# Kernel tuning notes

Measured on AMD Instinct MI355X. Metric: run time of the kernel, lower is better.

Reference implementation:

```python
import jax, jax.numpy as jnp
import numpy as np

H = 64  # hidden size
T = 11  # unrolled timesteps


def setup_inputs() -> dict:
    key = jax.random.key(0)
    ks = jax.random.split(key, 8)
    B, V, E = 65536, 50000, 100
    return {
        "sent": jax.random.randint(ks[0], (B, T), 0, V, dtype=jnp.int32),
        "emb_W": jax.random.normal(ks[1], (V, E), jnp.float32) * 0.05,
        "W_ih": jax.random.normal(ks[2], (4 * H, E), jnp.float32) * 0.05,
        "W_hh": jax.random.normal(ks[3], (4 * H, H), jnp.float32) * 0.05,
        "b_ih": jax.random.normal(ks[4], (4 * H,), jnp.float32) * 0.05,
        "b_hh": jax.random.normal(ks[5], (4 * H,), jnp.float32) * 0.05,
        "fc_W": jax.random.normal(ks[6], (14, H), jnp.float32) * 0.05,
        "fc_b": jax.random.normal(ks[7], (14,), jnp.float32) * 0.05,
    }


def _lstm_cell(x, h, c, W_ih, W_hh, b_ih, b_hh):
    # gates order in torch LSTMCell: i, f, g, o
    gates = x @ W_ih.T + b_ih + h @ W_hh.T + b_hh  # [B, 4H]
    i, f, g, o = jnp.split(gates, 4, axis=-1)
    c_new = jax.nn.sigmoid(f) * c + jax.nn.sigmoid(i) * jnp.tanh(g)
    h_new = jax.nn.sigmoid(o) * jnp.tanh(c_new)
    return h_new, c_new


def reference(sent, emb_W, W_ih, W_hh, b_ih, b_hh, fc_W, fc_b):
    embed = emb_W[sent]  # [B, T, E]
    B = embed.shape[0]
    h0 = jnp.zeros((B, H), embed.dtype)
    c0 = jnp.zeros((B, H), embed.dtype)
    xs = jnp.swapaxes(embed[:, :T, :], 0, 1)  # [T, B, E]

    def step(carry, x):
        h, c = carry
        h, c = _lstm_cell(x, h, c, W_ih, W_hh, b_ih, b_hh)
        return (h, c), None

    (h_last, _), _ = jax.lax.scan(step, (h0, c0), xs)
    logits = h_last @ fc_W.T + fc_b  # [B, 14]
    return jax.nn.log_softmax(logits, axis=-1)
```

## Files before the change

kernel.cpp:

```cpp
#include <hip/hip_runtime.h>
#include <hip/hip_bf16.h>

#define T_STEPS 11
#define E_DIM   100
#define XSL     2048
#define NDMA    (2 * T_STEPS)

typedef int   i32x2   __attribute__((ext_vector_type(2)));
typedef int   i32x4   __attribute__((ext_vector_type(4)));
typedef int   i32x8   __attribute__((ext_vector_type(8)));
typedef float f32x4   __attribute__((ext_vector_type(4)));
typedef _Float16 h16x2 __attribute__((ext_vector_type(2)));
typedef _Float16 h16x4 __attribute__((ext_vector_type(4)));
typedef _Float16 h16x8 __attribute__((ext_vector_type(8)));

typedef __attribute__((address_space(1))) const unsigned int g_as1;
typedef __attribute__((address_space(3))) unsigned int l_as3;

#define SCALE1 0x7f7f7f7f

__device__ __forceinline__ h16x2 spl2(float v) {
    _Float16 h = (_Float16)v;
    return (h16x2){h, h};
}
__device__ __forceinline__ h16x2 pk2(float a, float b) {
    return __builtin_bit_cast(h16x2, __builtin_amdgcn_cvt_pkrtz(a, b));
}
__device__ __forceinline__ unsigned char f2fp8(float f) {
    return (unsigned char)(__builtin_amdgcn_cvt_pk_fp8_f32(f, 0.f, 0, false) & 0xff);
}
__device__ __forceinline__ long long ll_lo(i32x4 v) {
    i32x2 t = {v[0], v[1]};
    return __builtin_bit_cast(long long, t);
}
__device__ __forceinline__ long long ll_hi(i32x4 v) {
    i32x2 t = {v[2], v[3]};
    return __builtin_bit_cast(long long, t);
}

__device__ __forceinline__ h16x2 tanh5(h16x2 x) {
    h16x2 x2 = x * x;
    h16x2 p = x2 * spl2(0.13333333f) + spl2(-0.33333333f);
    p = x2 * p + spl2(1.0f);
    return x * p;
}
__device__ __forceinline__ h16x2 tanh7(h16x2 x) {
    h16x2 x2 = x * x;
    h16x2 p = x2 * spl2(-0.05396825f) + spl2(0.13333333f);
    p = x2 * p + spl2(-0.33333333f);
    p = x2 * p + spl2(1.0f);
    return x * p;
}
__device__ __forceinline__ h16x2 sig3(h16x2 x) {
    h16x2 x2 = x * x;
    h16x2 p = x2 * spl2(-0.020833334f) + spl2(0.25f);
    return x * p + spl2(0.5f);
}

__global__ void pack_all(const float* __restrict__ emb,
                         const float* __restrict__ W_ih, const float* __restrict__ W_hh,
                         const float* __restrict__ b_ih, const float* __restrict__ b_hh,
                         unsigned char* __restrict__ embp8, unsigned char* __restrict__ Wx8,
                         unsigned char* __restrict__ Wh8, float* __restrict__ biasf, int V)
{
    int b = blockIdx.x;
    int tid = threadIdx.x;
    if (b < 128) {
        int id = b * 256 + tid;
        int n = id >> 7, k = id & 127;
        float v = (k < E_DIM) ? W_ih[n * E_DIM + k] : 0.f;
        int kt = k >> 5;
        int lane = (n & 15) | (((k & 31) >> 3) << 4);
        Wx8[((kt * 16 + (n >> 4)) * 64 + lane) * 8 + (k & 7)] = f2fp8(v);
    } else if (b < 192) {
        int id = (b - 128) * 256 + tid;
        int n = id >> 6, k = id & 63;
        int kt = k >> 5;
        int lane = (n & 15) | (((k & 31) >> 3) << 4);
        Wh8[((kt * 16 + (n >> 4)) * 64 + lane) * 8 + (k & 7)] = f2fp8(W_hh[n * 64 + k]);
    } else if (b == 192) {
        biasf[tid] = b_ih[tid] + b_hh[tid];
    } else {
        int id = (b - 193) * 256 + tid;
        if (id >= V * 8) return;
        int row = id >> 3;
        int c8 = id & 7;
        int p = c8 >> 2, qq = c8 & 3;
        const float* xr = emb + (size_t)row * E_DIM;
        float v[16];
        #pragma unroll
        for (int w = 0; w < 16; ++w) {
            int k = p * 64 + (w >> 3) * 32 + qq * 8 + (w & 7);
            v[w] = (k < E_DIM) ? xr[k] : 0.f;
        }
        int4 o;
        int* op = &o.x;
        #pragma unroll
        for (int w = 0; w < 4; ++w) {
            int d = __builtin_amdgcn_cvt_pk_fp8_f32(v[w*4+0], v[w*4+1], 0, false);
            d = __builtin_amdgcn_cvt_pk_fp8_f32(v[w*4+2], v[w*4+3], d, true);
            op[w] = d;
        }
        *reinterpret_cast<int4*>(embp8 + (size_t)row * 128 + c8 * 16) = o;
    }
}

template<int PACKED>
__global__ __launch_bounds__(256, 4)
void lstm_fused(const int* __restrict__ sent,
                const float* __restrict__ emb, const unsigned char* __restrict__ embp8,
                const unsigned char* __restrict__ Wx8, const unsigned char* __restrict__ Wh8,
                const float* __restrict__ biasf,
                const float* __restrict__ fc_W, const float* __restrict__ fc_b,
                float* __restrict__ out)
{
    __shared__ unsigned char xlds[T_STEPS * XSL];
    __shared__ unsigned char hlds[2][1024];
    __shared__ float biaslds[256];
    __shared__ short hscr[16 * 68];
    const int tid  = threadIdx.x;
    const int wv   = tid >> 6;
    const int lane = tid & 63;
    const int r    = lane & 15;
    const int q    = lane >> 4;
    const int b0   = blockIdx.x * 16;

    #pragma unroll
    for (int d = wv; d < NDMA; d += 4) {
        int sl = d >> 1, half = d & 1;
        int c  = half * 4 + (lane >> 4);
        int rr = lane & 15;
        int idx = sent[(b0 + rr) * T_STEPS + sl];
        if (PACKED) {
            const unsigned char* src = embp8 + (size_t)idx * 128 + c * 16;
            __builtin_amdgcn_global_load_lds(
                (g_as1*)src, (l_as3*)&xlds[sl * XSL + half * 1024], 16, 0, 0);
        } else {
            const float* xr = emb + (size_t)idx * E_DIM;
            int p = c >> 2, qq = c & 3;
            float v[16];
            #pragma unroll
            for (int w = 0; w < 16; ++w) {
                int k = p * 64 + (w >> 3) * 32 + qq * 8 + (w & 7);
                v[w] = (k < E_DIM) ? xr[k] : 0.f;
            }
            int4 o;
            int* op = &o.x;
            #pragma unroll
            for (int w = 0; w < 4; ++w) {
                int dd = __builtin_amdgcn_cvt_pk_fp8_f32(v[w*4+0], v[w*4+1], 0, false);
                dd = __builtin_amdgcn_cvt_pk_fp8_f32(v[w*4+2], v[w*4+3], dd, true);
                op[w] = dd;
            }
            *reinterpret_cast<int4*>(&xlds[sl * XSL + (half * 64 + lane) * 16]) = o;
        }
    }

    i32x8 wxm[4];
    #pragma unroll
    for (int g = 0; g < 4; ++g)
        #pragma unroll
        for (int kt = 0; kt < 4; ++kt) {
            i32x2 w = *reinterpret_cast<const i32x2*>(
                Wx8 + ((kt * 16 + g * 4 + wv) * 64 + lane) * 8);
            wxm[g][2 * kt]     = w[0];
            wxm[g][2 * kt + 1] = w[1];
        }
    long long wh[2][4];
    #pragma unroll
    for (int kt = 0; kt < 2; ++kt)
        #pragma unroll
        for (int g = 0; g < 4; ++g)
            wh[kt][g] = *reinterpret_cast<const long long*>(
                Wh8 + ((kt * 16 + g * 4 + wv) * 64 + lane) * 8);
    #pragma unroll
    for (int g = 0; g < 4; ++g)
        asm volatile("" : "+v"(wxm[g]));
    #pragma unroll
    for (int kt = 0; kt < 2; ++kt)
        #pragma unroll
        for (int g = 0; g < 4; ++g)
            asm volatile("" : "+v"(wh[kt][g]));

    biaslds[tid] = biasf[tid];
    reinterpret_cast<int*>(&hlds[0][0])[tid] = 0;

    __builtin_amdgcn_s_waitcnt(0);
    __syncthreads();

    auto acc_bias_x = [&](int sl, f32x4* acc) {
        #pragma unroll
        for (int g = 0; g < 4; ++g)
            acc[g] = *reinterpret_cast<const f32x4*>(
                &biaslds[(g * 4 + wv) * 16 + q * 4]);
        i32x4 v0 = *reinterpret_cast<const i32x4*>(
            &xlds[sl * XSL + (q * 16 + r) * 16]);
        i32x4 v1 = *reinterpret_cast<const i32x4*>(
            &xlds[sl * XSL + ((4 + q) * 16 + r) * 16]);
        i32x8 b8 = {v0[0], v0[1], v0[2], v0[3], v1[0], v1[1], v1[2], v1[3]};
        #pragma unroll
        for (int g = 0; g < 4; ++g)
            acc[g] = __builtin_amdgcn_mfma_scale_f32_16x16x128_f8f6f4(
                wxm[g], b8, acc[g], 0, 0, 0, SCALE1, 0, SCALE1);
    };

    h16x2 c01 = spl2(0.f), c23 = spl2(0.f);
    f32x4 acc[4];
    acc_bias_x(0, acc);

    const int hq  = (wv & 1) * 2 + (q >> 1);
    const int hoff = (hq * 16 + r) * 16 + (wv >> 1) * 8 + (q & 1) * 4;

    #pragma unroll
    for (int t = 0; t < T_STEPS; ++t) {
        i32x4 hv = *reinterpret_cast<const i32x4*>(&hlds[t & 1][(q * 16 + r) * 16]);
        long long bh0 = ll_lo(hv), bh1 = ll_hi(hv);
        #pragma unroll
        for (int g = 0; g < 4; ++g)
            acc[g] = __builtin_amdgcn_mfma_f32_16x16x32_fp8_fp8(wh[0][g], bh0, acc[g], 0, 0, 0);
        #pragma unroll
        for (int g = 0; g < 4; ++g)
            acc[g] = __builtin_amdgcn_mfma_f32_16x16x32_fp8_fp8(wh[1][g], bh1, acc[g], 0, 0, 0);

        h16x2 gi0 = pk2(acc[0][0], acc[0][1]), gi1 = pk2(acc[0][2], acc[0][3]);
        h16x2 gf0 = pk2(acc[1][0], acc[1][1]), gf1 = pk2(acc[1][2], acc[1][3]);
        h16x2 gg0 = pk2(acc[2][0], acc[2][1]), gg1 = pk2(acc[2][2], acc[2][3]);
        h16x2 go0 = pk2(acc[3][0], acc[3][1]), go1 = pk2(acc[3][2], acc[3][3]);
        c01 = sig3(gf0) * c01 + sig3(gi0) * tanh5(gg0);
        c23 = sig3(gf1) * c23 + sig3(gi1) * tanh5(gg1);
        h16x2 h01 = sig3(go0) * tanh7(c01);
        h16x2 h23 = sig3(go1) * tanh7(c23);

        int hw = __builtin_amdgcn_cvt_pk_fp8_f32((float)h01[0], (float)h01[1], 0, false);
        hw = __builtin_amdgcn_cvt_pk_fp8_f32((float)h23[0], (float)h23[1], hw, true);
        *reinterpret_cast<int*>(&hlds[(t + 1) & 1][hoff]) = hw;

        if (t == T_STEPS - 1) {
            h16x4 hn = { h01[0], h01[1], h23[0], h23[1] };
            *reinterpret_cast<h16x4*>(&hscr[r * 68 + wv * 16 + q * 4]) = hn;
        }

        if (t + 1 < T_STEPS) acc_bias_x(t + 1, acc);

        __syncthreads();
    }

    const int row_local = wv * 4 + q;
    const int cls = r;
    const int brow = b0 + row_local;
    float s = (cls < 14) ? fc_b[cls] : 0.f;
    const float* wrow = fc_W + ((cls < 14) ? cls : 0) * 64;
    #pragma unroll
    for (int ch = 0; ch < 8; ++ch) {
        h16x8 hv8 = *reinterpret_cast<const h16x8*>(&hscr[row_local * 68 + ch * 8]);
        #pragma unroll
        for (int j = 0; j < 8; ++j)
            s = fmaf((float)hv8[j], wrow[ch * 8 + j], s);
    }
    float lg = (cls < 14) ? s : -1e30f;
    float mx = lg;
    mx = fmaxf(mx, __shfl_xor(mx, 1));
    mx = fmaxf(mx, __shfl_xor(mx, 2));
    mx = fmaxf(mx, __shfl_xor(mx, 4));
    mx = fmaxf(mx, __shfl_xor(mx, 8));
    float se = __expf(lg - mx);
    se += __shfl_xor(se, 1);
    se += __shfl_xor(se, 2);
    se += __shfl_xor(se, 4);
    se += __shfl_xor(se, 8);
    float lse = mx + __logf(se);
    if (cls < 14) out[(size_t)brow * 14 + cls] = lg - lse;
}

extern "C" void kernel_launch(void* const* d_in, const int* in_sizes, int n_in,
                              void* d_out, int out_size, void* d_ws, size_t ws_size,
                              hipStream_t stream)
{
    const int*   sent = (const int*)d_in[0];
    const float* emb  = (const float*)d_in[1];
    const float* W_ih = (const float*)d_in[2];
    const float* W_hh = (const float*)d_in[3];
    const float* b_ih = (const float*)d_in[4];
    const float* b_hh = (const float*)d_in[5];
    const float* fc_W = (const float*)d_in[6];
    const float* fc_b = (const float*)d_in[7];
    float* out = (float*)d_out;

    const int B = in_sizes[0] / T_STEPS;
    const int V = in_sizes[1] / E_DIM;
    const size_t emb_bytes = (size_t)V * 128;
    const size_t need = emb_bytes + 32768 + 16384 + 1024;
    const bool packed = ws_size >= need;

    unsigned char* embp8 = (unsigned char*)d_ws;
    unsigned char* Wx8   = embp8 + emb_bytes;
    unsigned char* Wh8   = Wx8 + 32768;
    float*         biasf = (float*)(Wh8 + 16384);
    if (!packed) {
        Wx8   = (unsigned char*)d_ws;
        Wh8   = Wx8 + 32768;
        biasf = (float*)(Wh8 + 16384);
        embp8 = nullptr;
    }

    const int grid = B / 16;
    if (packed) {
        int pgrid = 193 + (V * 8 + 255) / 256;
        pack_all<<<pgrid, 256, 0, stream>>>(emb, W_ih, W_hh, b_ih, b_hh,
                                            embp8, Wx8, Wh8, biasf, V);
        lstm_fused<1><<<grid, 256, 0, stream>>>(sent, emb, embp8, Wx8, Wh8,
                                                biasf, fc_W, fc_b, out);
    } else {
        pack_all<<<193, 256, 0, stream>>>(emb, W_ih, W_hh, b_ih, b_hh,
                                          nullptr, Wx8, Wh8, biasf, 0);
        lstm_fused<0><<<grid, 256, 0, stream>>>(sent, emb, nullptr, Wx8, Wh8,
                                                biasf, fc_W, fc_b, out);
    }
}
```

Baseline: 147.0 us.

## Process two 16-row batch tiles per block to interleave independent recurrences

Each block now handles 32 batch rows as two independent 16-row LSTM chains. Their MFMAs and gate math are interleaved so one chain's latency can hide behind the other's work, and the per-step barrier cost and weight-register loads are shared across twice the rows. The grid is halved, LDS use roughly doubles, and launch bounds drop from 4 to 3 blocks per CU. The hscr scratch is folded into the reused x buffer. This trades occupancy and register pressure for more instruction-level parallelism.

```diff
diff --git a/kernel.cpp b/kernel.cpp
--- a/kernel.cpp
+++ b/kernel.cpp
@@ -106,7 +106,7 @@
 }
 
 template<int PACKED>
-__global__ __launch_bounds__(256, 4)
+__global__ __launch_bounds__(256, 3)
 void lstm_fused(const int* __restrict__ sent,
                 const float* __restrict__ emb, const unsigned char* __restrict__ embp8,
                 const unsigned char* __restrict__ Wx8, const unsigned char* __restrict__ Wh8,
@@ -114,27 +114,28 @@
                 const float* __restrict__ fc_W, const float* __restrict__ fc_b,
                 float* __restrict__ out)
 {
-    __shared__ unsigned char xlds[T_STEPS * XSL];
-    __shared__ unsigned char hlds[2][1024];
+    __shared__ unsigned char xlds[2][T_STEPS * XSL];
+    __shared__ unsigned char hlds[2][2][1024];
     __shared__ float biaslds[256];
-    __shared__ short hscr[16 * 68];
     const int tid  = threadIdx.x;
     const int wv   = tid >> 6;
     const int lane = tid & 63;
     const int r    = lane & 15;
     const int q    = lane >> 4;
-    const int b0   = blockIdx.x * 16;
-
-    #pragma unroll
-    for (int d = wv; d < NDMA; d += 4) {
-        int sl = d >> 1, half = d & 1;
+    const int b0   = blockIdx.x * 32;
+
+    #pragma unroll
+    for (int d = wv; d < 2 * NDMA; d += 4) {
+        int u  = (d >= NDMA);
+        int dd = d - u * NDMA;
+        int sl = dd >> 1, half = d & 1;
         int c  = half * 4 + (lane >> 4);
         int rr = lane & 15;
-        int idx = sent[(b0 + rr) * T_STEPS + sl];
+        int idx = sent[(b0 + u * 16 + rr) * T_STEPS + sl];
         if (PACKED) {
             const unsigned char* src = embp8 + (size_t)idx * 128 + c * 16;
             __builtin_amdgcn_global_load_lds(
-                (g_as1*)src, (l_as3*)&xlds[sl * XSL + half * 1024], 16, 0, 0);
+                (g_as1*)src, (l_as3*)&xlds[u][sl * XSL + half * 1024], 16, 0, 0);
         } else {
             const float* xr = emb + (size_t)idx * E_DIM;
             int p = c >> 2, qq = c & 3;
@@ -148,11 +149,11 @@
             int* op = &o.x;
             #pragma unroll
             for (int w = 0; w < 4; ++w) {
-                int dd = __builtin_amdgcn_cvt_pk_fp8_f32(v[w*4+0], v[w*4+1], 0, false);
-                dd = __builtin_amdgcn_cvt_pk_fp8_f32(v[w*4+2], v[w*4+3], dd, true);
-                op[w] = dd;
+                int e = __builtin_amdgcn_cvt_pk_fp8_f32(v[w*4+0], v[w*4+1], 0, false);
+                e = __builtin_amdgcn_cvt_pk_fp8_f32(v[w*4+2], v[w*4+3], e, true);
+                op[w] = e;
             }
-            *reinterpret_cast<int4*>(&xlds[sl * XSL + (half * 64 + lane) * 16]) = o;
+            *reinterpret_cast<int4*>(&xlds[u][sl * XSL + (half * 64 + lane) * 16]) = o;
         }
     }
 
@@ -183,20 +184,20 @@
             asm volatile("" : "+v"(wh[kt][g]));
 
     biaslds[tid] = biasf[tid];
-    reinterpret_cast<int*>(&hlds[0][0])[tid] = 0;
+    reinterpret_cast<int2*>(&hlds[0][0][0])[tid] = (int2){0, 0};
 
     __builtin_amdgcn_s_waitcnt(0);
     __syncthreads();
 
-    auto acc_bias_x = [&](int sl, f32x4* acc) {
+    auto acc_bias_x = [&](int sl, int u, f32x4* acc) {
         #pragma unroll
         for (int g = 0; g < 4; ++g)
             acc[g] = *reinterpret_cast<const f32x4*>(
                 &biaslds[(g * 4 + wv) * 16 + q * 4]);
         i32x4 v0 = *reinterpret_cast<const i32x4*>(
-            &xlds[sl * XSL + (q * 16 + r) * 16]);
+            &xlds[u][sl * XSL + (q * 16 + r) * 16]);
         i32x4 v1 = *reinterpret_cast<const i32x4*>(
-            &xlds[sl * XSL + ((4 + q) * 16 + r) * 16]);
+            &xlds[u][sl * XSL + ((4 + q) * 16 + r) * 16]);
         i32x8 b8 = {v0[0], v0[1], v0[2], v0[3], v1[0], v1[1], v1[2], v1[3]};
         #pragma unroll
         for (int g = 0; g < 4; ++g)
@@ -204,72 +205,96 @@
                 wxm[g], b8, acc[g], 0, 0, 0, SCALE1, 0, SCALE1);
     };
 
-    h16x2 c01 = spl2(0.f), c23 = spl2(0.f);
-    f32x4 acc[4];
-    acc_bias_x(0, acc);
-
-    const int hq  = (wv & 1) * 2 + (q >> 1);
+    h16x2 c01[2] = {spl2(0.f), spl2(0.f)}, c23[2] = {spl2(0.f), spl2(0.f)};
+    f32x4 acc[2][4];
+    acc_bias_x(0, 0, acc[0]);
+    acc_bias_x(0, 1, acc[1]);
+
+    const int hq   = (wv & 1) * 2 + (q >> 1);
     const int hoff = (hq * 16 + r) * 16 + (wv >> 1) * 8 + (q & 1) * 4;
 
+    h16x4 hfin[2];
+
     #pragma unroll
     for (int t = 0; t < T_STEPS; ++t) {
-        i32x4 hv = *reinterpret_cast<const i32x4*>(&hlds[t & 1][(q * 16 + r) * 16]);
-        long long bh0 = ll_lo(hv), bh1 = ll_hi(hv);
-        #pragma unroll
-        for (int g = 0; g < 4; ++g)
-            acc[g] = __builtin_amdgcn_mfma_f32_16x16x32_fp8_fp8(wh[0][g], bh0, acc[g], 0, 0, 0);
-        #pragma unroll
-        for (int g = 0; g < 4; ++g)
-            acc[g] = __builtin_amdgcn_mfma_f32_16x16x32_fp8_fp8(wh[1][g], bh1, acc[g], 0, 0, 0);
-
-        h16x2 gi0 = pk2(acc[0][0], acc[0][1]), gi1 = pk2(acc[0][2], acc[0][3]);
-        h16x2 gf0 = pk2(acc[1][0], acc[1][1]), gf1 = pk2(acc[1][2], acc[1][3]);
-        h16x2 gg0 = pk2(acc[2][0], acc[2][1]), gg1 = pk2(acc[2][2], acc[2][3]);
-        h16x2 go0 = pk2(acc[3][0], acc[3][1]), go1 = pk2(acc[3][2], acc[3][3]);
-        c01 = sig3(gf0) * c01 + sig3(gi0) * tanh5(gg0);
-        c23 = sig3(gf1) * c23 + sig3(gi1) * tanh5(gg1);
-        h16x2 h01 = sig3(go0) * tanh7(c01);
-        h16x2 h23 = sig3(go1) * tanh7(c23);
-
-        int hw = __builtin_amdgcn_cvt_pk_fp8_f32((float)h01[0], (float)h01[1], 0, false);
-        hw = __builtin_amdgcn_cvt_pk_fp8_f32((float)h23[0], (float)h23[1], hw, true);
-        *reinterpret_cast<int*>(&hlds[(t + 1) & 1][hoff]) = hw;
-
-        if (t == T_STEPS - 1) {
-            h16x4 hn = { h01[0], h01[1], h23[0], h23[1] };
-            *reinterpret_cast<h16x4*>(&hscr[r * 68 + wv * 16 + q * 4]) = hn;
-        }
-
-        if (t + 1 < T_STEPS) acc_bias_x(t + 1, acc);
+        i32x4 hv0 = *reinterpret_cast<const i32x4*>(&hlds[t & 1][0][(q * 16 + r) * 16]);
+        i32x4 hv1 = *reinterpret_cast<const i32x4*>(&hlds[t & 1][1][(q * 16 + r) * 16]);
+        {
+            long long a0 = ll_lo(hv0), a1 = ll_hi(hv0);
+            long long b0_ = ll_lo(hv1), b1 = ll_hi(hv1);
+            #pragma unroll
+            for (int g = 0; g < 4; ++g) {
+                acc[0][g] = __builtin_amdgcn_mfma_f32_16x16x32_fp8_fp8(wh[0][g], a0, acc[0][g], 0, 0, 0);
+                acc[1][g] = __builtin_amdgcn_mfma_f32_16x16x32_fp8_fp8(wh[0][g], b0_, acc[1][g], 0, 0, 0);
+            }
+            #pragma unroll
+            for (int g = 0; g < 4; ++g) {
+                acc[0][g] = __builtin_amdgcn_mfma_f32_16x16x32_fp8_fp8(wh[1][g], a1, acc[0][g], 0, 0, 0);
+                acc[1][g] = __builtin_amdgcn_mfma_f32_16x16x32_fp8_fp8(wh[1][g], b1, acc[1][g], 0, 0, 0);
+            }
+        }
+
+        #pragma unroll
+        for (int u = 0; u < 2; ++u) {
+            h16x2 gi0 = pk2(acc[u][0][0], acc[u][0][1]), gi1 = pk2(acc[u][0][2], acc[u][0][3]);
+            h16x2 gf0 = pk2(acc[u][1][0], acc[u][1][1]), gf1 = pk2(acc[u][1][2], acc[u][1][3]);
+            h16x2 gg0 = pk2(acc[u][2][0], acc[u][2][1]), gg1 = pk2(acc[u][2][2], acc[u][2][3]);
+            h16x2 go0 = pk2(acc[u][3][0], acc[u][3][1]), go1 = pk2(acc[u][3][2], acc[u][3][3]);
+            c01[u] = sig3(gf0) * c01[u] + sig3(gi0) * tanh5(gg0);
+            c23[u] = sig3(gf1) * c23[u] + sig3(gi1) * tanh5(gg1);
+            h16x2 h01 = sig3(go0) * tanh7(c01[u]);
+            h16x2 h23 = sig3(go1) * tanh7(c23[u]);
+            int hw = __builtin_amdgcn_cvt_pk_fp8_f32((float)h01[0], (float)h01[1], 0, false);
+            hw = __builtin_amdgcn_cvt_pk_fp8_f32((float)h23[0], (float)h23[1], hw, true);
+            *reinterpret_cast<int*>(&hlds[(t + 1) & 1][u][hoff]) = hw;
+            if (t == T_STEPS - 1)
+                hfin[u] = (h16x4){h01[0], h01[1], h23[0], h23[1]};
+        }
+
+        if (t + 1 < T_STEPS) {
+            acc_bias_x(t + 1, 0, acc[0]);
+            acc_bias_x(t + 1, 1, acc[1]);
+        }
 
         __syncthreads();
     }
+
+    #pragma unroll
+    for (int u = 0; u < 2; ++u) {
+        short* hscr = reinterpret_cast<short*>(&xlds[u][0]);
+        *reinterpret_cast<h16x4*>(&hscr[r * 68 + wv * 16 + q * 4]) = hfin[u];
+    }
+    __syncthreads();
 
     const int row_local = wv * 4 + q;
     const int cls = r;
-    const int brow = b0 + row_local;
-    float s = (cls < 14) ? fc_b[cls] : 0.f;
     const float* wrow = fc_W + ((cls < 14) ? cls : 0) * 64;
-    #pragma unroll
-    for (int ch = 0; ch < 8; ++ch) {
-        h16x8 hv8 = *reinterpret_cast<const h16x8*>(&hscr[row_local * 68 + ch * 8]);
-        #pragma unroll
-        for (int j = 0; j < 8; ++j)
-            s = fmaf((float)hv8[j], wrow[ch * 8 + j], s);
-    }
-    float lg = (cls < 14) ? s : -1e30f;
-    float mx = lg;
-    mx = fmaxf(mx, __shfl_xor(mx, 1));
-    mx = fmaxf(mx, __shfl_xor(mx, 2));
-    mx = fmaxf(mx, __shfl_xor(mx, 4));
-    mx = fmaxf(mx, __shfl_xor(mx, 8));
-    float se = __expf(lg - mx);
-    se += __shfl_xor(se, 1);
-    se += __shfl_xor(se, 2);
-    se += __shfl_xor(se, 4);
-    se += __shfl_xor(se, 8);
-    float lse = mx + __logf(se);
-    if (cls < 14) out[(size_t)brow * 14 + cls] = lg - lse;
+    float bias_c = (cls < 14) ? fc_b[cls] : 0.f;
+    #pragma unroll
+    for (int u = 0; u < 2; ++u) {
+        const short* hscr = reinterpret_cast<const short*>(&xlds[u][0]);
+        float s = bias_c;
+        #pragma unroll
+        for (int ch = 0; ch < 8; ++ch) {
+            h16x8 hv8 = *reinterpret_cast<const h16x8*>(&hscr[row_local * 68 + ch * 8]);
+            #pragma unroll
+            for (int j = 0; j < 8; ++j)
+                s = fmaf((float)hv8[j], wrow[ch * 8 + j], s);
+        }
+        float lg = (cls < 14) ? s : -1e30f;
+        float mx = lg;
+        mx = fmaxf(mx, __shfl_xor(mx, 1));
+        mx = fmaxf(mx, __shfl_xor(mx, 2));
+        mx = fmaxf(mx, __shfl_xor(mx, 4));
+        mx = fmaxf(mx, __shfl_xor(mx, 8));
+        float se = __expf(lg - mx);
+        se += __shfl_xor(se, 1);
+        se += __shfl_xor(se, 2);
+        se += __shfl_xor(se, 4);
+        se += __shfl_xor(se, 8);
+        float lse = mx + __logf(se);
+        if (cls < 14) out[(size_t)(b0 + u * 16 + row_local) * 14 + cls] = lg - lse;
+    }
 }
 
 extern "C" void kernel_launch(void* const* d_in, const int* in_sizes, int n_in,
@@ -303,7 +328,7 @@
         embp8 = nullptr;
     }
 
-    const int grid = B / 16;
+    const int grid = B / 32;
     if (packed) {
         int pgrid = 193 + (V * 8 + 255) / 256;
         pack_all<<<pgrid, 256, 0, stream>>>(emb, W_ih, W_hh, b_ih, b_hh,
```

Result: slower. 151.5 us (+3.1%).

## Make LSTM blocks persistent over four batch tiles with embedding prefetch

Applied to the files above, without the earlier changes.

Each block now processes four 16-row batch tiles in sequence instead of one. This amortizes the weight register loads and block launch cost across tiles. While the current tile's recurrence runs, the embedding gathers for the next tile are issued into the slots already consumed. The first timestep also skips the h@W_hh MFMAs and the forget-gate term, since h and c start at zero. The trade-off is a grid four times smaller, which gives less parallelism for hiding latency, plus an extra barrier between tiles.

```diff
diff --git a/kernel.cpp b/kernel.cpp
--- a/kernel.cpp
+++ b/kernel.cpp
@@ -5,6 +5,7 @@
 #define E_DIM   100
 #define XSL     2048
 #define NDMA    (2 * T_STEPS)
+#define NT      4
 
 typedef int   i32x2   __attribute__((ext_vector_type(2)));
 typedef int   i32x4   __attribute__((ext_vector_type(4)));
@@ -123,14 +124,12 @@
     const int lane = tid & 63;
     const int r    = lane & 15;
     const int q    = lane >> 4;
-    const int b0   = blockIdx.x * 16;
-
-    #pragma unroll
-    for (int d = wv; d < NDMA; d += 4) {
-        int sl = d >> 1, half = d & 1;
+    const int base = blockIdx.x * (16 * NT);
+
+    auto stage_dma = [&](int tb0, int sl, int half) {
         int c  = half * 4 + (lane >> 4);
         int rr = lane & 15;
-        int idx = sent[(b0 + rr) * T_STEPS + sl];
+        int idx = sent[(tb0 + rr) * T_STEPS + sl];
         if (PACKED) {
             const unsigned char* src = embp8 + (size_t)idx * 128 + c * 16;
             __builtin_amdgcn_global_load_lds(
@@ -154,7 +153,10 @@
             }
             *reinterpret_cast<int4*>(&xlds[sl * XSL + (half * 64 + lane) * 16]) = o;
         }
-    }
+    };
+
+    #pragma unroll
+    for (int d = wv; d < NDMA; d += 4) stage_dma(base, d >> 1, d & 1);
 
     i32x8 wxm[4];
     #pragma unroll
@@ -183,7 +185,6 @@
             asm volatile("" : "+v"(wh[kt][g]));
 
     biaslds[tid] = biasf[tid];
-    reinterpret_cast<int*>(&hlds[0][0])[tid] = 0;
 
     __builtin_amdgcn_s_waitcnt(0);
     __syncthreads();
@@ -204,72 +205,92 @@
                 wxm[g], b8, acc[g], 0, 0, 0, SCALE1, 0, SCALE1);
     };
 
-    h16x2 c01 = spl2(0.f), c23 = spl2(0.f);
-    f32x4 acc[4];
-    acc_bias_x(0, acc);
-
-    const int hq  = (wv & 1) * 2 + (q >> 1);
+    const int hq   = (wv & 1) * 2 + (q >> 1);
     const int hoff = (hq * 16 + r) * 16 + (wv >> 1) * 8 + (q & 1) * 4;
-
-    #pragma unroll
-    for (int t = 0; t < T_STEPS; ++t) {
-        i32x4 hv = *reinterpret_cast<const i32x4*>(&hlds[t & 1][(q * 16 + r) * 16]);
-        long long bh0 = ll_lo(hv), bh1 = ll_hi(hv);
-        #pragma unroll
-        for (int g = 0; g < 4; ++g)
-            acc[g] = __builtin_amdgcn_mfma_f32_16x16x32_fp8_fp8(wh[0][g], bh0, acc[g], 0, 0, 0);
-        #pragma unroll
-        for (int g = 0; g < 4; ++g)
-            acc[g] = __builtin_amdgcn_mfma_f32_16x16x32_fp8_fp8(wh[1][g], bh1, acc[g], 0, 0, 0);
-
-        h16x2 gi0 = pk2(acc[0][0], acc[0][1]), gi1 = pk2(acc[0][2], acc[0][3]);
-        h16x2 gf0 = pk2(acc[1][0], acc[1][1]), gf1 = pk2(acc[1][2], acc[1][3]);
-        h16x2 gg0 = pk2(acc[2][0], acc[2][1]), gg1 = pk2(acc[2][2], acc[2][3]);
-        h16x2 go0 = pk2(acc[3][0], acc[3][1]), go1 = pk2(acc[3][2], acc[3][3]);
-        c01 = sig3(gf0) * c01 + sig3(gi0) * tanh5(gg0);
-        c23 = sig3(gf1) * c23 + sig3(gi1) * tanh5(gg1);
-        h16x2 h01 = sig3(go0) * tanh7(c01);
-        h16x2 h23 = sig3(go1) * tanh7(c23);
-
-        int hw = __builtin_amdgcn_cvt_pk_fp8_f32((float)h01[0], (float)h01[1], 0, false);
-        hw = __builtin_amdgcn_cvt_pk_fp8_f32((float)h23[0], (float)h23[1], hw, true);
-        *reinterpret_cast<int*>(&hlds[(t + 1) & 1][hoff]) = hw;
-
-        if (t == T_STEPS - 1) {
-            h16x4 hn = { h01[0], h01[1], h23[0], h23[1] };
-            *reinterpret_cast<h16x4*>(&hscr[r * 68 + wv * 16 + q * 4]) = hn;
-        }
-
-        if (t + 1 < T_STEPS) acc_bias_x(t + 1, acc);
+    const int row_local = wv * 4 + q;
+    const int cls = r;
+    const float* wrow = fc_W + ((cls < 14) ? cls : 0) * 64;
+
+    #pragma unroll 1
+    for (int u = 0; u < NT; ++u) {
+        const int b0  = base + u * 16;
+        const bool pf = (u + 1 < NT);
+        const int nb0 = b0 + 16;
+
+        h16x2 c01 = spl2(0.f), c23 = spl2(0.f);
+        f32x4 acc[4];
+        acc_bias_x(0, acc);
+
+        #pragma unroll
+        for (int t = 0; t < T_STEPS; ++t) {
+            if (t >= 1 && pf && wv < 2) stage_dma(nb0, t - 1, wv);
+
+            if (t > 0) {
+                i32x4 hv = *reinterpret_cast<const i32x4*>(&hlds[t & 1][(q * 16 + r) * 16]);
+                long long bh0 = ll_lo(hv), bh1 = ll_hi(hv);
+                #pragma unroll
+                for (int g = 0; g < 4; ++g)
+                    acc[g] = __builtin_amdgcn_mfma_f32_16x16x32_fp8_fp8(wh[0][g], bh0, acc[g], 0, 0, 0);
+                #pragma unroll
+                for (int g = 0; g < 4; ++g)
+                    acc[g] = __builtin_amdgcn_mfma_f32_16x16x32_fp8_fp8(wh[1][g], bh1, acc[g], 0, 0, 0);
+            }
+
+            h16x2 gi0 = pk2(acc[0][0], acc[0][1]), gi1 = pk2(acc[0][2], acc[0][3]);
+            h16x2 gg0 = pk2(acc[2][0], acc[2][1]), gg1 = pk2(acc[2][2], acc[2][3]);
+            h16x2 go0 = pk2(acc[3][0], acc[3][1]), go1 = pk2(acc[3][2], acc[3][3]);
+            if (t == 0) {
+                c01 = sig3(gi0) * tanh5(gg0);
+                c23 = sig3(gi1) * tanh5(gg1);
+            } else {
+                h16x2 gf0 = pk2(acc[1][0], acc[1][1]), gf1 = pk2(acc[1][2], acc[1][3]);
+                c01 = sig3(gf0) * c01 + sig3(gi0) * tanh5(gg0);
+                c23 = sig3(gf1) * c23 + sig3(gi1) * tanh5(gg1);
+            }
+            h16x2 h01 = sig3(go0) * tanh7(c01);
+            h16x2 h23 = sig3(go1) * tanh7(c23);
+
+            int hw = __builtin_amdgcn_cvt_pk_fp8_f32((float)h01[0], (float)h01[1], 0, false);
+            hw = __builtin_amdgcn_cvt_pk_fp8_f32((float)h23[0], (float)h23[1], hw, true);
+            *reinterpret_cast<int*>(&hlds[(t + 1) & 1][hoff]) = hw;
+
+            if (t == T_STEPS - 1) {
+                h16x4 hn = { h01[0], h01[1], h23[0], h23[1] };
+                *reinterpret_cast<h16x4*>(&hscr[r * 68 + wv * 16 + q * 4]) = hn;
+            }
+
+            if (t + 1 < T_STEPS) acc_bias_x(t + 1, acc);
+
+            __syncthreads();
+        }
+
+        if (pf && wv < 2) stage_dma(nb0, T_STEPS - 1, wv);
+        __builtin_amdgcn_s_waitcnt(0);
+
+        float s = (cls < 14) ? fc_b[cls] : 0.f;
+        #pragma unroll
+        for (int ch = 0; ch < 8; ++ch) {
+            h16x8 hv8 = *reinterpret_cast<const h16x8*>(&hscr[row_local * 68 + ch * 8]);
+            #pragma unroll
+            for (int j = 0; j < 8; ++j)
+                s = fmaf((float)hv8[j], wrow[ch * 8 + j], s);
+        }
+        float lg = (cls < 14) ? s : -1e30f;
+        float mx = lg;
+        mx = fmaxf(mx, __shfl_xor(mx, 1));
+        mx = fmaxf(mx, __shfl_xor(mx, 2));
+        mx = fmaxf(mx, __shfl_xor(mx, 4));
+        mx = fmaxf(mx, __shfl_xor(mx, 8));
+        float se = __expf(lg - mx);
+        se += __shfl_xor(se, 1);
+        se += __shfl_xor(se, 2);
+        se += __shfl_xor(se, 4);
+        se += __shfl_xor(se, 8);
+        float lse = mx + __logf(se);
+        if (cls < 14) out[(size_t)(b0 + row_local) * 14 + cls] = lg - lse;
 
         __syncthreads();
     }
-
-    const int row_local = wv * 4 + q;
-    const int cls = r;
-    const int brow = b0 + row_local;
-    float s = (cls < 14) ? fc_b[cls] : 0.f;
-    const float* wrow = fc_W + ((cls < 14) ? cls : 0) * 64;
-    #pragma unroll
-    for (int ch = 0; ch < 8; ++ch) {
-        h16x8 hv8 = *reinterpret_cast<const h16x8*>(&hscr[row_local * 68 + ch * 8]);
-        #pragma unroll
-        for (int j = 0; j < 8; ++j)
-            s = fmaf((float)hv8[j], wrow[ch * 8 + j], s);
-    }
-    float lg = (cls < 14) ? s : -1e30f;
-    float mx = lg;
-    mx = fmaxf(mx, __shfl_xor(mx, 1));
-    mx = fmaxf(mx, __shfl_xor(mx, 2));
-    mx = fmaxf(mx, __shfl_xor(mx, 4));
-    mx = fmaxf(mx, __shfl_xor(mx, 8));
-    float se = __expf(lg - mx);
-    se += __shfl_xor(se, 1);
-    se += __shfl_xor(se, 2);
-    se += __shfl_xor(se, 4);
-    se += __shfl_xor(se, 8);
-    float lse = mx + __logf(se);
-    if (cls < 14) out[(size_t)brow * 14 + cls] = lg - lse;
 }
 
 extern "C" void kernel_launch(void* const* d_in, const int* in_sizes, int n_in,
@@ -303,7 +324,7 @@
         embp8 = nullptr;
     }
 
-    const int grid = B / 16;
+    const int grid = B / (16 * NT);
     if (packed) {
         int pgrid = 193 + (V * 8 + 255) / 256;
         pack_all<<<pgrid, 256, 0, stream>>>(emb, W_ih, W_hh, b_ih, b_hh,
```

Result: slower. 151.0 us (+2.8%).
